# Performance work log

Hardware: AMD Instinct MI355X
Metric: run time of the kernel (lower is better)

## Reference

```python
import jax, jax.numpy as jnp
import numpy as np


def softmax_kernel(data, projection, is_query, eps=1e-4):
    # data: [b,h,n,d], projection: [m,d]
    d = data.shape[-1]
    data_normalizer = d ** -0.25
    ratio = projection.shape[0] ** -0.5
    data_dash = jnp.einsum('bhnd,md->bhnm', data_normalizer * data, projection)
    diag_data = (data ** 2).sum(axis=-1) * 0.5 * (data_normalizer ** 2)  # [b,h,n]
    diag_data = diag_data[..., None]
    if is_query:
        m = jnp.max(data_dash, axis=-1, keepdims=True)  # per-query max
    else:
        m = jnp.max(data_dash)  # global max over all keys
    return ratio * (jnp.exp(data_dash - diag_data - m) + eps)


def linear_attention(q, k, v):
    # q,k: [b,h,n,m] feature maps; v: [b,h,n,e]
    D_inv = 1.0 / jnp.einsum('bhnm,bhm->bhn', q, k.sum(axis=-2))
    context = jnp.einsum('bhnm,bhne->bhme', k, v)
    return jnp.einsum('bhme,bhnm,bhn->bhne', context, q, D_inv)


def setup_inputs() -> dict:
    key = jax.random.key(0)
    k1, k2, k3, k4 = jax.random.split(key, 4)
    B, H, N, D, M = 4, 16, 4096, 64, 256
    # gaussian orthogonal random matrix (scaling=0): 4 orthogonal DxD blocks,
    # rows rescaled by norms of gaussian rows
    blocks = []
    kk = k4
    for _ in range(M // D):
        kk, sub = jax.random.split(kk)
        g = jax.random.normal(sub, (D, D), dtype=jnp.float32)
        qmat, _ = jnp.linalg.qr(g)
        blocks.append(qmat.T)
    final = jnp.concatenate(blocks, axis=0)  # [M, D]
    kk, sub = jax.random.split(kk)
    multiplier = jnp.linalg.norm(jax.random.normal(sub, (M, D), dtype=jnp.float32), axis=1)
    proj = multiplier[:, None] * final
    return {
        'q': jax.random.normal(k1, (B, H, N, D), dtype=jnp.float32),
        'k': jax.random.normal(k2, (B, H, N, D), dtype=jnp.float32),
        'v': jax.random.normal(k3, (B, H, N, D), dtype=jnp.float32),
        'projection': proj,
    }


def reference(q, k, v, projection):
    q_prime = softmax_kernel(q, projection, is_query=True)
    k_prime = softmax_kernel(k, projection, is_query=False)
    return linear_attention(q_prime, k_prime, v)
```

## Files before the change

kernel.cpp:

```cpp
#include <hip/hip_runtime.h>
#include <hip/hip_bf16.h>


#define BH    64
#define NSEQ  4096
#define DD    64
#define MM    256
#define DN    0.35355339059327373f
#define RATIO 0.0625f
#define EPS   1e-4f
#define NSEG  8

#define CTX_OFF  0
#define KSUM_OFF (BH*MM*DD)
#define VSUM_OFF (KSUM_OFF + BH*MM)
#define MG_OFF   (VSUM_OFF + BH*DD)
#define CTX_SLICE (BH*MM*DD)

typedef __attribute__((ext_vector_type(8)))  short bf16x8;
typedef __attribute__((ext_vector_type(16))) float f32x16;

#define MFMA(a,b,c) __builtin_amdgcn_mfma_f32_32x32x16_bf16((a),(b),(c),0,0,0)
#define PATROW(r,h) ((((r)&3) + 8*((r)>>2)) + 4*(h))

__device__ __forceinline__ unsigned short f2bf(float x) {
    unsigned u = __float_as_uint(x);
    return (unsigned short)((u + 0x7fffu + ((u >> 16) & 1u)) >> 16);
}
__device__ __forceinline__ void split8(const float* x, bf16x8& hv, bf16x8& lv) {
#pragma unroll
    for (int i = 0; i < 8; ++i) {
        unsigned short hb = f2bf(x[i]);
        float hf = __uint_as_float(((unsigned)hb) << 16);
        hv[i] = (short)hb;
        lv[i] = (short)f2bf(x[i] - hf);
    }
}
__device__ __forceinline__ bf16x8 hi8(const float* x) {
    union { short s[8]; bf16x8 v; } r;
#pragma unroll
    for (int i = 0; i < 8; ++i) r.s[i] = (short)f2bf(x[i]);
    return r.v;
}
__device__ __forceinline__ unsigned ford(float f) {
    unsigned u = __float_as_uint(f);
    return (u & 0x80000000u) ? ~u : (u | 0x80000000u);
}
__device__ __forceinline__ float ford_inv(unsigned u) {
    return (u & 0x80000000u) ? __uint_as_float(u & 0x7fffffffu) : __uint_as_float(~u);
}
__device__ __forceinline__ unsigned pkbf(float lo, float hi) {
    union { __hip_bfloat162 b2; unsigned u; } cvt;
    cvt.b2 = __float22bfloat162_rn(make_float2(lo, hi));
    return cvt.u;
}
template<int BASE>
__device__ __forceinline__ bf16x8 repack8(const f32x16& a, int h) {
    unsigned X0 = pkbf(a[BASE+0], a[BASE+1]);
    unsigned X1 = pkbf(a[BASE+2], a[BASE+3]);
    unsigned Y0 = pkbf(a[BASE+4], a[BASE+5]);
    unsigned Y1 = pkbf(a[BASE+6], a[BASE+7]);
    unsigned tX0 = (unsigned)__shfl_xor((int)X0, 32);
    unsigned tX1 = (unsigned)__shfl_xor((int)X1, 32);
    unsigned tY0 = (unsigned)__shfl_xor((int)Y0, 32);
    unsigned tY1 = (unsigned)__shfl_xor((int)Y1, 32);
    union { unsigned w[4]; bf16x8 v; } r;
    r.w[0] = h ? tY0 : X0;
    r.w[1] = h ? tY1 : X1;
    r.w[2] = h ? Y0 : tX0;
    r.w[3] = h ? Y1 : tX1;
    return r.v;
}

__global__ __launch_bounds__(512, 2)
void keys_kernel(const float* __restrict__ kg, const float* __restrict__ vg,
                 const float* __restrict__ pg, float* __restrict__ ws,
                 float* __restrict__ outp)
{
    __shared__ __align__(16) short kfh[2][64*64];
    __shared__ __align__(16) short kfl[2][64*64];
    __shared__ __align__(16) short vT [2][64*64];
    __shared__ float diagl[2][64];
    __shared__ float vswr[8][64];

    const int tid  = threadIdx.x;
    const int wv   = tid >> 6;
    const int lane = tid & 63;
    const int l31  = lane & 31;
    const int h    = lane >> 5;
    const int bh   = blockIdx.x >> 3;
    const int seg  = blockIdx.x & 7;

    bf16x8 pBh[4];
    {
        const int m = 32*wv + l31;
#pragma unroll
        for (int ks = 0; ks < 4; ++ks) {
            const int d0 = 16*ks + 8*h;
            float x[8];
            *(float4*)&x[0] = *(const float4*)(pg + m*64 + d0);
            *(float4*)&x[4] = *(const float4*)(pg + m*64 + d0 + 4);
            pBh[ks] = hi8(x);
        }
    }

    f32x16 cacc0, cacc1;
#pragma unroll
    for (int i = 0; i < 16; ++i) { cacc0[i] = 0.f; cacc1[i] = 0.f; }
    float ksacc = 0.f, mloc = -3e38f;
    float vsacc[8];
#pragma unroll
    for (int i = 0; i < 8; ++i) vsacc[i] = 0.f;

    auto stage = [&](int ch, int p) {
        const int n = tid >> 3, dg = tid & 7, d0 = dg*8;
        const size_t base = ((size_t)(bh*NSEQ + seg*512 + ch*64 + n)) * DD;
        float x[8];
        *(float4*)&x[0] = *(const float4*)(kg + base + d0);
        *(float4*)&x[4] = *(const float4*)(kg + base + d0 + 4);
        float ss = 0.f;
#pragma unroll
        for (int i = 0; i < 8; ++i) { x[i] *= DN; ss += x[i]*x[i]; }
        ss += __shfl_xor(ss, 1); ss += __shfl_xor(ss, 2); ss += __shfl_xor(ss, 4);
        if (dg == 0) diagl[p][n] = 0.5f * ss;
        bf16x8 hv, lv; split8(x, hv, lv);
        const int ofs = dg*512 + ((n*8) ^ (dg*8));
        *(bf16x8*)&kfh[p][ofs] = hv;
        *(bf16x8*)&kfl[p][ofs] = lv;
        float y[8];
        *(float4*)&y[0] = *(const float4*)(vg + base + d0);
        *(float4*)&y[4] = *(const float4*)(vg + base + d0 + 4);
#pragma unroll
        for (int i = 0; i < 8; ++i) {
            vsacc[i] += y[i];
            vT[p][(d0+i)*64 + (n ^ ((i ^ dg) << 3))] = (short)f2bf(y[i]);
        }
    };

    stage(0, 0);
    __syncthreads();
    int p = 0;
    for (int ch = 0; ch < 8; ++ch) {
        if (ch < 7) stage(ch+1, p^1);

        f32x16 s0, s1;
#pragma unroll
        for (int i = 0; i < 16; ++i) { s0[i] = 0.f; s1[i] = 0.f; }
#pragma unroll
        for (int ks = 0; ks < 4; ++ks) {
            const int dg2 = ks*2 + h;
            const int ofs = dg2*512 + ((l31*8) ^ (dg2*8));
            bf16x8 a0h = *(const bf16x8*)&kfh[p][ofs];
            bf16x8 a0l = *(const bf16x8*)&kfl[p][ofs];
            bf16x8 a1h = *(const bf16x8*)&kfh[p][ofs + 256];
            bf16x8 a1l = *(const bf16x8*)&kfl[p][ofs + 256];
            s0 = MFMA(a0h, pBh[ks], s0);
            s1 = MFMA(a1h, pBh[ks], s1);
            s0 = MFMA(a0l, pBh[ks], s0);
            s1 = MFMA(a1l, pBh[ks], s1);
        }

#pragma unroll
        for (int r = 0; r < 16; ++r) {
            const int n0 = PATROW(r, h);
            mloc = fmaxf(mloc, s0[r]);
            const float w0 = __expf(s0[r] - diagl[p][n0]);
            s0[r] = w0; ksacc += w0;
            mloc = fmaxf(mloc, s1[r]);
            const float w1 = __expf(s1[r] - diagl[p][32 + n0]);
            s1[r] = w1; ksacc += w1;
        }

        bf16x8 wfr[4];
        wfr[0] = repack8<0>(s0, h);
        wfr[1] = repack8<8>(s0, h);
        wfr[2] = repack8<0>(s1, h);
        wfr[3] = repack8<8>(s1, h);

#pragma unroll
        for (int ks = 0; ks < 4; ++ks) {
            const int nb = 16*ks + 8*h;
            const int e0 = l31, e1 = l31 + 32;
            bf16x8 b0 = *(const bf16x8*)&vT[p][e0*64 + (nb ^ (((e0&7) ^ (e0>>3))<<3))];
            bf16x8 b1 = *(const bf16x8*)&vT[p][e1*64 + (nb ^ (((e1&7) ^ (e1>>3))<<3))];
            cacc0 = MFMA(wfr[ks], b0, cacc0);
            cacc1 = MFMA(wfr[ks], b1, cacc1);
        }
        __syncthreads();
        p ^= 1;
    }

    ksacc += __shfl_xor(ksacc, 32);
    if (h == 0) atomicAdd(&ws[KSUM_OFF + bh*MM + 32*wv + l31], ksacc);

#pragma unroll
    for (int m = 1; m <= 32; m <<= 1) mloc = fmaxf(mloc, __shfl_xor(mloc, m));
    if (lane == 0) atomicMax((unsigned*)&ws[MG_OFF], ford(mloc));

    {
        float* cb = outp + (size_t)(seg*BH + bh) * (MM*DD);
#pragma unroll
        for (int r = 0; r < 16; ++r) {
            const int m = 32*wv + PATROW(r, h);
            cb[m*64 + l31]      = cacc0[r];
            cb[m*64 + l31 + 32] = cacc1[r];
        }
    }

#pragma unroll
    for (int i = 0; i < 8; ++i) {
        float v = vsacc[i];
        v += __shfl_xor(v, 8); v += __shfl_xor(v, 16); v += __shfl_xor(v, 32);
        vsacc[i] = v;
    }
    if (lane < 8) {
#pragma unroll
        for (int i = 0; i < 8; ++i) vswr[wv][lane*8 + i] = vsacc[i];
    }
    __syncthreads();
    if (tid < 64) {
        float s = 0.f;
#pragma unroll
        for (int w = 0; w < 8; ++w) s += vswr[w][tid];
        atomicAdd(&ws[VSUM_OFF + bh*DD + tid], s);
    }
}

__global__ __launch_bounds__(512)
void reduce_kernel(const float* __restrict__ outp, float* __restrict__ ws)
{
    const int idx = blockIdx.x * 512 + threadIdx.x;
    const float4* o4 = (const float4*)outp;
    float4 s = o4[idx];
#pragma unroll
    for (int sl = 1; sl < NSEG; ++sl) {
        float4 t = o4[sl*(CTX_SLICE/4) + idx];
        s.x += t.x; s.y += t.y; s.z += t.z; s.w += t.w;
    }
    ((float4*)(ws + CTX_OFF))[idx] = s;
}

__global__ __launch_bounds__(512, 2)
void query_kernel(const float* __restrict__ qg, const float* __restrict__ pg,
                  const float* __restrict__ ws, float* __restrict__ out)
{
    __shared__ __align__(16) short pfh[MM*DD];
    __shared__ __align__(16) short ctxb[32*64*8];
    __shared__ float ksuml[MM];
    __shared__ float ctxsuml[DD];
    __shared__ float ksumsuml;
    __shared__ float epsl[8][32];
    __shared__ float denl[8][32];

    const int tid  = threadIdx.x;
    const int wv   = tid >> 6;
    const int lane = tid & 63;
    const int l31  = lane & 31;
    const int h    = lane >> 5;
    const int bh   = blockIdx.x >> 3;
    const int seg  = blockIdx.x & 7;

    const float mg = ford_inv(*(const unsigned*)&ws[MG_OFF]);
    const float cs = RATIO * __expf(-mg);
    const float ce = RATIO * EPS;

    if (tid < DD) ctxsuml[tid] = 0.f;
    if (tid == 0) ksumsuml = 0.f;
    __syncthreads();

    {
        const int m = tid >> 1, dh = tid & 1;
#pragma unroll
        for (int b = 0; b < 4; ++b) {
            const int d0 = dh*32 + b*8;
            float x[8];
            *(float4*)&x[0] = *(const float4*)(pg + m*64 + d0);
            *(float4*)&x[4] = *(const float4*)(pg + m*64 + d0 + 4);
            const int g = ((m>>5)*4 + (d0>>4))*2 + ((d0>>3)&1);
            *(bf16x8*)&pfh[(g*32 + (m&31))*8] = hi8(x);
        }
    }
#pragma unroll
    for (int it = 0; it < 4; ++it) {
        const int gid = it*512 + tid;
        const int g = gid >> 6, e = gid & 63;
        const int mb = (g>>1)*16 + (g&1)*8;
        const float vs = ws[VSUM_OFF + bh*DD + e];
        float part = 0.f;
        union { short s[8]; bf16x8 v; } tmp;
#pragma unroll
        for (int j = 0; j < 8; ++j) {
            const float x = cs*ws[CTX_OFF + (size_t)bh*(MM*DD) + (mb+j)*64 + e] + ce*vs;
            part += x;
            tmp.s[j] = (short)f2bf(x);
        }
        *(bf16x8*)&ctxb[(g*64 + e)*8] = tmp.v;
        atomicAdd(&ctxsuml[e], part);
    }
    if (tid < 256) {
        const float kt = cs*ws[KSUM_OFF + bh*MM + tid] + ce*(float)NSEQ;
        ksuml[tid] = kt;
        atomicAdd(&ksumsuml, kt);
    }
    __syncthreads();

    const float cs0 = ctxsuml[l31];
    const float cs1 = ctxsuml[l31 + 32];
    const float kss = ksumsuml;

    for (int ch = 0; ch < 2; ++ch) {
        const int rown = seg*512 + ch*256 + wv*32;
        const size_t gn = (size_t)(bh*NSEQ + rown + l31);

        bf16x8 qbh[4], qbl[4];
        float ss = 0.f;
#pragma unroll
        for (int ks = 0; ks < 4; ++ks) {
            const int d0 = 16*ks + 8*h;
            float x[8];
            *(float4*)&x[0] = *(const float4*)(qg + gn*64 + d0);
            *(float4*)&x[4] = *(const float4*)(qg + gn*64 + d0 + 4);
#pragma unroll
            for (int i = 0; i < 8; ++i) { x[i] *= DN; ss += x[i]*x[i]; }
            split8(x, qbh[ks], qbl[ks]);
        }
        const float diag = 0.5f * (ss + __shfl_xor(ss, 32));

        f32x16 n0, n1;
#pragma unroll
        for (int i = 0; i < 16; ++i) { n0[i] = 0.f; n1[i] = 0.f; }
        float den = 0.f, mx = -3e38f;
#pragma unroll
        for (int mt = 0; mt < 8; ++mt) {
            f32x16 s;
#pragma unroll
            for (int i = 0; i < 16; ++i) s[i] = 0.f;
#pragma unroll
            for (int ks = 0; ks < 4; ++ks) {
                const int g = (mt*4 + ks)*2 + h;
                bf16x8 ah = *(const bf16x8*)&pfh[(g*32 + l31)*8];
                s = MFMA(ah, qbh[ks], s);
                s = MFMA(ah, qbl[ks], s);
            }
#pragma unroll
            for (int r = 0; r < 16; ++r) mx = fmaxf(mx, s[r]);
#pragma unroll
            for (int r = 0; r < 16; ++r) {
                const float u = __expf(s[r] - diag);
                s[r] = u;
                den = fmaf(u, ksuml[mt*32 + PATROW(r, h)], den);
            }
            bf16x8 t0 = repack8<0>(s, h);
            bf16x8 t1 = repack8<8>(s, h);
            const int g0 = 4*mt + h, g1 = 4*mt + 2 + h;
            n0 = MFMA(t0, *(const bf16x8*)&ctxb[(g0*64 + l31)*8],      n0);
            n1 = MFMA(t0, *(const bf16x8*)&ctxb[(g0*64 + l31 + 32)*8], n1);
            n0 = MFMA(t1, *(const bf16x8*)&ctxb[(g1*64 + l31)*8],      n0);
            n1 = MFMA(t1, *(const bf16x8*)&ctxb[(g1*64 + l31 + 32)*8], n1);
        }

        mx  = fmaxf(mx, __shfl_xor(mx, 32));
        den += __shfl_xor(den, 32);
        const float epsp = EPS * __expf(mx);
        const float denf = den + epsp * kss;
        if (h == 0) { epsl[wv][l31] = epsp; denl[wv][l31] = denf; }
        asm volatile("s_waitcnt lgkmcnt(0)" ::: "memory");

#pragma unroll
        for (int r = 0; r < 16; ++r) {
            const int nn = PATROW(r, h);
            const float e1  = epsl[wv][nn];
            const float rdn = 1.0f / denl[wv][nn];
            float* op = out + ((size_t)(bh*NSEQ + rown + nn))*64;
            op[l31]      = (n0[r] + e1*cs0) * rdn;
            op[l31 + 32] = (n1[r] + e1*cs1) * rdn;
        }
    }
}

extern "C" void kernel_launch(void* const* d_in, const int* in_sizes, int n_in,
                              void* d_out, int out_size, void* d_ws, size_t ws_size,
                              hipStream_t stream)
{
    const float* q = (const float*)d_in[0];
    const float* k = (const float*)d_in[1];
    const float* v = (const float*)d_in[2];
    const float* p = (const float*)d_in[3];
    float* ws  = (float*)d_ws;
    float* out = (float*)d_out;

    (void)hipMemsetAsync((void*)(ws + KSUM_OFF),
                         0, (size_t)(BH*MM + BH*DD + 4) * sizeof(float), stream);
    keys_kernel<<<dim3(512), dim3(512), 0, stream>>>(k, v, p, ws, out);
    reduce_kernel<<<dim3(512), dim3(512), 0, stream>>>(out, ws);
    query_kernel<<<dim3(512), dim3(512), 0, stream>>>(q, p, ws, out);
}
```

Before: 157.8 us.

## Triple-buffer key staging and software-pipeline score GEMM with context MFMA

Moves shared buffers from double to triple buffering. The score GEMM for the next chunk now runs in the same phase as the context MFMAs of the current chunk, so the exp/max work overlaps with MFMA issue, and s_setprio is raised around the MFMA section. Diagonal values are now read as float4 vectors instead of scalar LDS loads. The third buffer adds LDS use, which may lower occupancy under launch_bounds(512,2), and the extra live accumulators raise register pressure.

New measurement: 155.5 us. Within noise of the previous version (-1.5%).

```diff
diff --git a/kernel.cpp b/kernel.cpp
--- a/kernel.cpp
+++ b/kernel.cpp
@@ -77,10 +77,10 @@
                  const float* __restrict__ pg, float* __restrict__ ws,
                  float* __restrict__ outp)
 {
-    __shared__ __align__(16) short kfh[2][64*64];
-    __shared__ __align__(16) short kfl[2][64*64];
-    __shared__ __align__(16) short vT [2][64*64];
-    __shared__ float diagl[2][64];
+    __shared__ __align__(16) short kfh[3][64*64];
+    __shared__ __align__(16) short kfl[3][64*64];
+    __shared__ __align__(16) short vT [3][64*64];
+    __shared__ float diagl[3][64];
     __shared__ float vswr[8][64];
 
     const int tid  = threadIdx.x;
@@ -112,7 +112,7 @@
 #pragma unroll
     for (int i = 0; i < 8; ++i) vsacc[i] = 0.f;
 
-    auto stage = [&](int ch, int p) {
+    auto stage = [&](int ch, int b) {
         const int n = tid >> 3, dg = tid & 7, d0 = dg*8;
         const size_t base = ((size_t)(bh*NSEQ + seg*512 + ch*64 + n)) * DD;
         float x[8];
@@ -122,72 +122,98 @@
 #pragma unroll
         for (int i = 0; i < 8; ++i) { x[i] *= DN; ss += x[i]*x[i]; }
         ss += __shfl_xor(ss, 1); ss += __shfl_xor(ss, 2); ss += __shfl_xor(ss, 4);
-        if (dg == 0) diagl[p][n] = 0.5f * ss;
+        if (dg == 0) diagl[b][n] = 0.5f * ss;
         bf16x8 hv, lv; split8(x, hv, lv);
         const int ofs = dg*512 + ((n*8) ^ (dg*8));
-        *(bf16x8*)&kfh[p][ofs] = hv;
-        *(bf16x8*)&kfl[p][ofs] = lv;
+        *(bf16x8*)&kfh[b][ofs] = hv;
+        *(bf16x8*)&kfl[b][ofs] = lv;
         float y[8];
         *(float4*)&y[0] = *(const float4*)(vg + base + d0);
         *(float4*)&y[4] = *(const float4*)(vg + base + d0 + 4);
 #pragma unroll
         for (int i = 0; i < 8; ++i) {
             vsacc[i] += y[i];
-            vT[p][(d0+i)*64 + (n ^ ((i ^ dg) << 3))] = (short)f2bf(y[i]);
+            vT[b][(d0+i)*64 + (n ^ ((i ^ dg) << 3))] = (short)f2bf(y[i]);
         }
     };
 
-    stage(0, 0);
-    __syncthreads();
-    int p = 0;
-    for (int ch = 0; ch < 8; ++ch) {
-        if (ch < 7) stage(ch+1, p^1);
-
-        f32x16 s0, s1;
-#pragma unroll
-        for (int i = 0; i < 16; ++i) { s0[i] = 0.f; s1[i] = 0.f; }
+    auto sgemm = [&](int b, f32x16& r0, f32x16& r1) {
+#pragma unroll
+        for (int i = 0; i < 16; ++i) { r0[i] = 0.f; r1[i] = 0.f; }
 #pragma unroll
         for (int ks = 0; ks < 4; ++ks) {
             const int dg2 = ks*2 + h;
             const int ofs = dg2*512 + ((l31*8) ^ (dg2*8));
-            bf16x8 a0h = *(const bf16x8*)&kfh[p][ofs];
-            bf16x8 a0l = *(const bf16x8*)&kfl[p][ofs];
-            bf16x8 a1h = *(const bf16x8*)&kfh[p][ofs + 256];
-            bf16x8 a1l = *(const bf16x8*)&kfl[p][ofs + 256];
-            s0 = MFMA(a0h, pBh[ks], s0);
-            s1 = MFMA(a1h, pBh[ks], s1);
-            s0 = MFMA(a0l, pBh[ks], s0);
-            s1 = MFMA(a1l, pBh[ks], s1);
-        }
-
-#pragma unroll
-        for (int r = 0; r < 16; ++r) {
-            const int n0 = PATROW(r, h);
-            mloc = fmaxf(mloc, s0[r]);
-            const float w0 = __expf(s0[r] - diagl[p][n0]);
-            s0[r] = w0; ksacc += w0;
-            mloc = fmaxf(mloc, s1[r]);
-            const float w1 = __expf(s1[r] - diagl[p][32 + n0]);
-            s1[r] = w1; ksacc += w1;
-        }
-
+            bf16x8 a0h = *(const bf16x8*)&kfh[b][ofs];
+            bf16x8 a0l = *(const bf16x8*)&kfl[b][ofs];
+            bf16x8 a1h = *(const bf16x8*)&kfh[b][ofs + 256];
+            bf16x8 a1l = *(const bf16x8*)&kfl[b][ofs + 256];
+            r0 = MFMA(a0h, pBh[ks], r0);
+            r1 = MFMA(a1h, pBh[ks], r1);
+            r0 = MFMA(a0l, pBh[ks], r0);
+            r1 = MFMA(a1l, pBh[ks], r1);
+        }
+    };
+
+    stage(0, 0);
+    __syncthreads();
+    f32x16 s0, s1;
+    sgemm(0, s0, s1);
+
+    for (int ch = 0; ch < 8; ++ch) {
+        const int bc = ch % 3, bn = (ch + 1) % 3;
+        if (ch < 7) stage(ch + 1, bn);
+
+        {
+            float kp = 0.f;
+#pragma unroll
+            for (int g = 0; g < 4; ++g) {
+                const float4 dq = *(const float4*)&diagl[bc][8*g + 4*h];
+                const float dd[4] = {dq.x, dq.y, dq.z, dq.w};
+#pragma unroll
+                for (int j = 0; j < 4; ++j) {
+                    const int r = 4*g + j;
+                    mloc = fmaxf(mloc, s0[r]);
+                    const float w = __expf(s0[r] - dd[j]);
+                    s0[r] = w; kp += w;
+                }
+            }
+#pragma unroll
+            for (int g = 0; g < 4; ++g) {
+                const float4 dq = *(const float4*)&diagl[bc][32 + 8*g + 4*h];
+                const float dd[4] = {dq.x, dq.y, dq.z, dq.w};
+#pragma unroll
+                for (int j = 0; j < 4; ++j) {
+                    const int r = 4*g + j;
+                    mloc = fmaxf(mloc, s1[r]);
+                    const float w = __expf(s1[r] - dd[j]);
+                    s1[r] = w; kp += w;
+                }
+            }
+            ksacc += kp;
+        }
         bf16x8 wfr[4];
         wfr[0] = repack8<0>(s0, h);
         wfr[1] = repack8<8>(s0, h);
         wfr[2] = repack8<0>(s1, h);
         wfr[3] = repack8<8>(s1, h);
 
+        __syncthreads();
+
+        __builtin_amdgcn_s_setprio(1);
+        f32x16 ns0, ns1;
+        if (ch < 7) sgemm(bn, ns0, ns1);
 #pragma unroll
         for (int ks = 0; ks < 4; ++ks) {
             const int nb = 16*ks + 8*h;
             const int e0 = l31, e1 = l31 + 32;
-            bf16x8 b0 = *(const bf16x8*)&vT[p][e0*64 + (nb ^ (((e0&7) ^ (e0>>3))<<3))];
-            bf16x8 b1 = *(const bf16x8*)&vT[p][e1*64 + (nb ^ (((e1&7) ^ (e1>>3))<<3))];
+            bf16x8 b0 = *(const bf16x8*)&vT[bc][e0*64 + (nb ^ (((e0&7) ^ (e0>>3))<<3))];
+            bf16x8 b1 = *(const bf16x8*)&vT[bc][e1*64 + (nb ^ (((e1&7) ^ (e1>>3))<<3))];
             cacc0 = MFMA(wfr[ks], b0, cacc0);
             cacc1 = MFMA(wfr[ks], b1, cacc1);
         }
-        __syncthreads();
-        p ^= 1;
+        __builtin_amdgcn_s_setprio(0);
+        if (ch < 7) { s0 = ns0; s1 = ns1; }
     }
 
     ksacc += __shfl_xor(ksacc, 32);
```

## Drop bf16 low-part split and software-pipeline keys kernel with 128-row chunks

Applied to the files above, without the earlier changes.

Removes the hi/lo bf16 split of the scaled keys and queries, so each projection GEMM uses a single bf16 MFMA pass instead of two. The keys kernel now stages 128-row chunks with wider per-thread loads. Its main loop is restructured so the score GEMM of one 64-row half overlaps the exp and context MFMAs of the other, with s_setprio hints added. This halves the projection MFMA work and LDS for keys, at the cost of lower precision in the exponent arguments, which could hurt accuracy.

After: 167.6 us. 1.06x slower.

```diff
diff --git a/kernel.cpp b/kernel.cpp
--- a/kernel.cpp
+++ b/kernel.cpp
@@ -26,15 +26,6 @@
 __device__ __forceinline__ unsigned short f2bf(float x) {
     unsigned u = __float_as_uint(x);
     return (unsigned short)((u + 0x7fffu + ((u >> 16) & 1u)) >> 16);
-}
-__device__ __forceinline__ void split8(const float* x, bf16x8& hv, bf16x8& lv) {
-#pragma unroll
-    for (int i = 0; i < 8; ++i) {
-        unsigned short hb = f2bf(x[i]);
-        float hf = __uint_as_float(((unsigned)hb) << 16);
-        hv[i] = (short)hb;
-        lv[i] = (short)f2bf(x[i] - hf);
-    }
 }
 __device__ __forceinline__ bf16x8 hi8(const float* x) {
     union { short s[8]; bf16x8 v; } r;
@@ -71,16 +62,16 @@
     r.w[3] = h ? Y1 : tX1;
     return r.v;
 }
+#define VSWZ(e) ((((e)&7) ^ ((e)>>3)) << 3)
 
 __global__ __launch_bounds__(512, 2)
 void keys_kernel(const float* __restrict__ kg, const float* __restrict__ vg,
                  const float* __restrict__ pg, float* __restrict__ ws,
                  float* __restrict__ outp)
 {
-    __shared__ __align__(16) short kfh[2][64*64];
-    __shared__ __align__(16) short kfl[2][64*64];
-    __shared__ __align__(16) short vT [2][64*64];
-    __shared__ float diagl[2][64];
+    __shared__ __align__(16) short kf[2][8*1024];
+    __shared__ __align__(16) short vT[2][64*128];
+    __shared__ float diagl[2][128];
     __shared__ float vswr[8][64];
 
     const int tid  = threadIdx.x;
@@ -108,86 +99,115 @@
 #pragma unroll
     for (int i = 0; i < 16; ++i) { cacc0[i] = 0.f; cacc1[i] = 0.f; }
     float ksacc = 0.f, mloc = -3e38f;
-    float vsacc[8];
-#pragma unroll
-    for (int i = 0; i < 8; ++i) vsacc[i] = 0.f;
-
-    auto stage = [&](int ch, int p) {
-        const int n = tid >> 3, dg = tid & 7, d0 = dg*8;
-        const size_t base = ((size_t)(bh*NSEQ + seg*512 + ch*64 + n)) * DD;
-        float x[8];
-        *(float4*)&x[0] = *(const float4*)(kg + base + d0);
-        *(float4*)&x[4] = *(const float4*)(kg + base + d0 + 4);
+    float vsacc[16];
+#pragma unroll
+    for (int i = 0; i < 16; ++i) vsacc[i] = 0.f;
+
+    auto stage = [&](int ch, int b) {
+        const int n = tid >> 2, q = tid & 3;
+        const size_t base = ((size_t)(bh*NSEQ + seg*512 + ch*128 + n)) * 64 + q*16;
+        float x[16], y[16];
+        *(float4*)&x[0]  = *(const float4*)(kg + base);
+        *(float4*)&x[4]  = *(const float4*)(kg + base + 4);
+        *(float4*)&x[8]  = *(const float4*)(kg + base + 8);
+        *(float4*)&x[12] = *(const float4*)(kg + base + 12);
+        *(float4*)&y[0]  = *(const float4*)(vg + base);
+        *(float4*)&y[4]  = *(const float4*)(vg + base + 4);
+        *(float4*)&y[8]  = *(const float4*)(vg + base + 8);
+        *(float4*)&y[12] = *(const float4*)(vg + base + 12);
         float ss = 0.f;
 #pragma unroll
-        for (int i = 0; i < 8; ++i) { x[i] *= DN; ss += x[i]*x[i]; }
-        ss += __shfl_xor(ss, 1); ss += __shfl_xor(ss, 2); ss += __shfl_xor(ss, 4);
-        if (dg == 0) diagl[p][n] = 0.5f * ss;
-        bf16x8 hv, lv; split8(x, hv, lv);
-        const int ofs = dg*512 + ((n*8) ^ (dg*8));
-        *(bf16x8*)&kfh[p][ofs] = hv;
-        *(bf16x8*)&kfl[p][ofs] = lv;
-        float y[8];
-        *(float4*)&y[0] = *(const float4*)(vg + base + d0);
-        *(float4*)&y[4] = *(const float4*)(vg + base + d0 + 4);
-#pragma unroll
-        for (int i = 0; i < 8; ++i) {
+        for (int i = 0; i < 16; ++i) { x[i] *= DN; ss += x[i]*x[i]; }
+        ss += __shfl_xor(ss, 1); ss += __shfl_xor(ss, 2);
+        if (q == 0) diagl[b][n] = 0.5f * ss;
+        const int dg0 = 2*q, dg1 = 2*q + 1;
+        *(bf16x8*)&kf[b][dg0*1024 + ((n*8) ^ (dg0*8))] = hi8(x);
+        *(bf16x8*)&kf[b][dg1*1024 + ((n*8) ^ (dg1*8))] = hi8(x + 8);
+#pragma unroll
+        for (int i = 0; i < 16; ++i) {
             vsacc[i] += y[i];
-            vT[p][(d0+i)*64 + (n ^ ((i ^ dg) << 3))] = (short)f2bf(y[i]);
+            const int e = q*16 + i;
+            vT[b][e*128 + (n ^ VSWZ(e))] = (short)f2bf(y[i]);
+        }
+    };
+
+    auto sgemm = [&](int b, int hf, f32x16& r0, f32x16& r1) {
+#pragma unroll
+        for (int i = 0; i < 16; ++i) { r0[i] = 0.f; r1[i] = 0.f; }
+#pragma unroll
+        for (int ks = 0; ks < 4; ++ks) {
+            const int dg = ks*2 + h;
+            const int ofs = dg*1024 + ((((64*hf) + l31)*8) ^ (dg*8));
+            bf16x8 a0 = *(const bf16x8*)&kf[b][ofs];
+            bf16x8 a1 = *(const bf16x8*)&kf[b][ofs + 256];
+            r0 = MFMA(a0, pBh[ks], r0);
+            r1 = MFMA(a1, pBh[ks], r1);
+        }
+    };
+
+    auto expack = [&](int b, int hf, f32x16& t0, f32x16& t1, bf16x8* wfr) {
+        float kp = 0.f;
+#pragma unroll
+        for (int g = 0; g < 4; ++g) {
+            const float4 dq0 = *(const float4*)&diagl[b][64*hf + 8*g + 4*h];
+            const float4 dq1 = *(const float4*)&diagl[b][64*hf + 32 + 8*g + 4*h];
+            const float d0[4] = {dq0.x, dq0.y, dq0.z, dq0.w};
+            const float d1[4] = {dq1.x, dq1.y, dq1.z, dq1.w};
+#pragma unroll
+            for (int j = 0; j < 4; ++j) {
+                const int r = 4*g + j;
+                mloc = fmaxf(mloc, t0[r]);
+                const float w0 = __expf(t0[r] - d0[j]);
+                t0[r] = w0; kp += w0;
+                mloc = fmaxf(mloc, t1[r]);
+                const float w1 = __expf(t1[r] - d1[j]);
+                t1[r] = w1; kp += w1;
+            }
+        }
+        ksacc += kp;
+        wfr[0] = repack8<0>(t0, h);
+        wfr[1] = repack8<8>(t0, h);
+        wfr[2] = repack8<0>(t1, h);
+        wfr[3] = repack8<8>(t1, h);
+    };
+
+    auto ctxg = [&](int b, int hf, const bf16x8* wfr) {
+#pragma unroll
+        for (int ks = 0; ks < 4; ++ks) {
+            const int nb = 64*hf + 16*ks + 8*h;
+            const int e0 = l31, e1 = l31 + 32;
+            bf16x8 b0 = *(const bf16x8*)&vT[b][e0*128 + (nb ^ VSWZ(e0))];
+            bf16x8 b1 = *(const bf16x8*)&vT[b][e1*128 + (nb ^ VSWZ(e1))];
+            cacc0 = MFMA(wfr[ks], b0, cacc0);
+            cacc1 = MFMA(wfr[ks], b1, cacc1);
         }
     };
 
     stage(0, 0);
     __syncthreads();
-    int p = 0;
-    for (int ch = 0; ch < 8; ++ch) {
-        if (ch < 7) stage(ch+1, p^1);
-
-        f32x16 s0, s1;
-#pragma unroll
-        for (int i = 0; i < 16; ++i) { s0[i] = 0.f; s1[i] = 0.f; }
-#pragma unroll
-        for (int ks = 0; ks < 4; ++ks) {
-            const int dg2 = ks*2 + h;
-            const int ofs = dg2*512 + ((l31*8) ^ (dg2*8));
-            bf16x8 a0h = *(const bf16x8*)&kfh[p][ofs];
-            bf16x8 a0l = *(const bf16x8*)&kfl[p][ofs];
-            bf16x8 a1h = *(const bf16x8*)&kfh[p][ofs + 256];
-            bf16x8 a1l = *(const bf16x8*)&kfl[p][ofs + 256];
-            s0 = MFMA(a0h, pBh[ks], s0);
-            s1 = MFMA(a1h, pBh[ks], s1);
-            s0 = MFMA(a0l, pBh[ks], s0);
-            s1 = MFMA(a1l, pBh[ks], s1);
-        }
-
-#pragma unroll
-        for (int r = 0; r < 16; ++r) {
-            const int n0 = PATROW(r, h);
-            mloc = fmaxf(mloc, s0[r]);
-            const float w0 = __expf(s0[r] - diagl[p][n0]);
-            s0[r] = w0; ksacc += w0;
-            mloc = fmaxf(mloc, s1[r]);
-            const float w1 = __expf(s1[r] - diagl[p][32 + n0]);
-            s1[r] = w1; ksacc += w1;
-        }
-
-        bf16x8 wfr[4];
-        wfr[0] = repack8<0>(s0, h);
-        wfr[1] = repack8<8>(s0, h);
-        wfr[2] = repack8<0>(s1, h);
-        wfr[3] = repack8<8>(s1, h);
-
-#pragma unroll
-        for (int ks = 0; ks < 4; ++ks) {
-            const int nb = 16*ks + 8*h;
-            const int e0 = l31, e1 = l31 + 32;
-            bf16x8 b0 = *(const bf16x8*)&vT[p][e0*64 + (nb ^ (((e0&7) ^ (e0>>3))<<3))];
-            bf16x8 b1 = *(const bf16x8*)&vT[p][e1*64 + (nb ^ (((e1&7) ^ (e1>>3))<<3))];
-            cacc0 = MFMA(wfr[ks], b0, cacc0);
-            cacc1 = MFMA(wfr[ks], b1, cacc1);
-        }
+    f32x16 sA0, sA1;
+    sgemm(0, 0, sA0, sA1);
+
+    for (int ch = 0; ch < 4; ++ch) {
+        const int bc = ch & 1, bn = bc ^ 1;
+        if (ch < 3) stage(ch + 1, bn);
+
+        bf16x8 wfrA[4];
+        expack(bc, 0, sA0, sA1, wfrA);
+        f32x16 sB0, sB1;
+        __builtin_amdgcn_s_setprio(1);
+        sgemm(bc, 1, sB0, sB1);
+        ctxg(bc, 0, wfrA);
+        __builtin_amdgcn_s_setprio(0);
+        bf16x8 wfrB[4];
+        expack(bc, 1, sB0, sB1, wfrB);
+        ctxg(bc, 1, wfrB);
         __syncthreads();
-        p ^= 1;
+        if (ch < 3) {
+            __builtin_amdgcn_s_setprio(1);
+            sgemm(bn, 0, sA0, sA1);
+            __builtin_amdgcn_s_setprio(0);
+        }
     }
 
     ksacc += __shfl_xor(ksacc, 32);
@@ -208,14 +228,15 @@
     }
 
 #pragma unroll
-    for (int i = 0; i < 8; ++i) {
+    for (int i = 0; i < 16; ++i) {
         float v = vsacc[i];
-        v += __shfl_xor(v, 8); v += __shfl_xor(v, 16); v += __shfl_xor(v, 32);
+        v += __shfl_xor(v, 4); v += __shfl_xor(v, 8);
+        v += __shfl_xor(v, 16); v += __shfl_xor(v, 32);
         vsacc[i] = v;
     }
-    if (lane < 8) {
-#pragma unroll
-        for (int i = 0; i < 8; ++i) vswr[wv][lane*8 + i] = vsacc[i];
+    if (lane < 4) {
+#pragma unroll
+        for (int i = 0; i < 16; ++i) vswr[wv][lane*16 + i] = vsacc[i];
     }
     __syncthreads();
     if (tid < 64) {
@@ -312,7 +333,7 @@
         const int rown = seg*512 + ch*256 + wv*32;
         const size_t gn = (size_t)(bh*NSEQ + rown + l31);
 
-        bf16x8 qbh[4], qbl[4];
+        bf16x8 qbh[4];
         float ss = 0.f;
 #pragma unroll
         for (int ks = 0; ks < 4; ++ks) {
@@ -322,7 +343,7 @@
             *(float4*)&x[4] = *(const float4*)(qg + gn*64 + d0 + 4);
 #pragma unroll
             for (int i = 0; i < 8; ++i) { x[i] *= DN; ss += x[i]*x[i]; }
-            split8(x, qbh[ks], qbl[ks]);
+            qbh[ks] = hi8(x);
         }
         const float diag = 0.5f * (ss + __shfl_xor(ss, 32));
 
@@ -340,7 +361,6 @@
                 const int g = (mt*4 + ks)*2 + h;
                 bf16x8 ah = *(const bf16x8*)&pfh[(g*32 + l31)*8];
                 s = MFMA(ah, qbh[ks], s);
-                s = MFMA(ah, qbl[ks], s);
             }
 #pragma unroll
             for (int r = 0; r < 16; ++r) mx = fmaxf(mx, s[r]);
```
